# Kernel optimization log

Measured on AMD Instinct MI355X. Metric: run time of the kernel, lower is better.

The kernel has to match this reference:

```python
import jax, jax.numpy as jnp
import numpy as np

N_FEATURES = 512
D_MODEL = 1024
BATCH = 256
LN_EPS = 1e-5


def setup_inputs() -> dict:
    key = jax.random.key(0)
    ks = jax.random.split(key, 8)
    x = jax.random.normal(ks[0], (BATCH, N_FEATURES), dtype=jnp.float32)
    prev_ca = jax.random.uniform(ks[1], (BATCH, D_MODEL), dtype=jnp.float32)
    # phase_proj: Linear(n_features, d_model)
    Wp = jax.random.normal(ks[2], (D_MODEL, N_FEATURES), dtype=jnp.float32) * (1.0 / np.sqrt(N_FEATURES))
    bp = jnp.zeros((D_MODEL,), dtype=jnp.float32)
    # ca_gate: Linear(d_model, d_model//2) + sigmoid
    Wg = jax.random.normal(ks[3], (D_MODEL // 2, D_MODEL), dtype=jnp.float32) * (1.0 / np.sqrt(D_MODEL))
    bg = jnp.zeros((D_MODEL // 2,), dtype=jnp.float32)
    # coupling matrix W (learned param, prev_W is None in default path)
    W = jax.random.normal(ks[4], (D_MODEL, D_MODEL), dtype=jnp.float32) * 0.01
    # LayerNorm params
    gamma = jnp.ones((D_MODEL,), dtype=jnp.float32)
    beta = jnp.zeros((D_MODEL,), dtype=jnp.float32)
    return {"x": x, "prev_ca": prev_ca, "Wp": Wp, "bp": bp, "Wg": Wg, "bg": bg, "W": W, "gamma": gamma, "beta": beta}


def _layernorm(h, gamma, beta):
    mu = jnp.mean(h, axis=-1, keepdims=True)
    var = jnp.mean(jnp.square(h - mu), axis=-1, keepdims=True)
    return (h - mu) * jax.lax.rsqrt(var + LN_EPS) * gamma + beta


def reference(x, prev_ca, Wp, bp, Wg, bg, W, gamma, beta):
    # phi: [B, d]
    phi = x @ Wp.T + bp
    # pairwise phase coherence |cos(phi_i - phi_j)| -> mean over j: [B, d]
    coherence = jnp.abs(jnp.cos(phi[:, :, None] - phi[:, None, :]))  # [B, d, d]
    ca_update = jnp.mean(coherence, axis=2)
    ca = prev_ca * 0.95 + ca_update * 0.05
    # calcium gate: sigmoid(Linear(d -> d//2)), tiled to d
    ca_gate = jax.nn.sigmoid(ca @ Wg.T + bg)  # [B, d//2]
    coupled = phi @ W  # [B, d]
    ca_gate_full = jnp.concatenate([ca_gate, ca_gate], axis=1)  # [B, d]
    features = coupled * ca_gate_full
    features = _layernorm(features + phi, gamma, beta)
    return features, ca, W
```

## Files before the change

kernel.cpp:

```cpp
#include <hip/hip_runtime.h>
#include <math.h>

#define BATCH   256
#define NFEAT   512
#define DMODEL  1024
#define DHALF   512
#define LN_EPS  1e-5f
#define LDSK    68

typedef float f2 __attribute__((ext_vector_type(2)));
typedef float f4 __attribute__((ext_vector_type(4)));

template <int M, int N, int K, int SPLIT, bool B_NT, bool BIAS, bool SIG>
__global__ __launch_bounds__(256) void gemm64_kernel(
    const float* __restrict__ A, const float* __restrict__ B,
    const float* __restrict__ bias, float* __restrict__ C) {
  __shared__ __align__(16) float As[64 * LDSK];
  __shared__ __align__(16) float Bs[64 * LDSK];
  constexpr int KC = K / SPLIT;
  constexpr int NT = KC / 64;
  const int bm  = blockIdx.x * 64;
  const int bn  = blockIdx.y * 64;
  const int kb  = blockIdx.z * KC;
  const int tid = threadIdx.x;
  const int tx  = tid & 15;
  const int ty  = tid >> 4;
  const int r16 = tid >> 4;
  const int c4  = tid & 15;

  f4 ar[4], br[4];

  auto load_tile = [&](int t) {
#pragma unroll
    for (int jj = 0; jj < 4; ++jj) {
      const int row = r16 + jj * 16;
      ar[jj] = *(const f4*)(&A[(size_t)(bm + row) * K + kb + t * 64 + c4 * 4]);
      if (B_NT)
        br[jj] = *(const f4*)(&B[(size_t)(bn + row) * K + kb + t * 64 + c4 * 4]);
      else
        br[jj] = *(const f4*)(&B[(size_t)(kb + t * 64 + row) * N + bn + c4 * 4]);
    }
  };
  auto store_tile = [&]() {
#pragma unroll
    for (int jj = 0; jj < 4; ++jj) {
      const int row = r16 + jj * 16;
      As[(c4 * 4 + 0) * LDSK + row] = ar[jj].x;
      As[(c4 * 4 + 1) * LDSK + row] = ar[jj].y;
      As[(c4 * 4 + 2) * LDSK + row] = ar[jj].z;
      As[(c4 * 4 + 3) * LDSK + row] = ar[jj].w;
      if (B_NT) {
        Bs[(c4 * 4 + 0) * LDSK + row] = br[jj].x;
        Bs[(c4 * 4 + 1) * LDSK + row] = br[jj].y;
        Bs[(c4 * 4 + 2) * LDSK + row] = br[jj].z;
        Bs[(c4 * 4 + 3) * LDSK + row] = br[jj].w;
      } else {
        *(f4*)(&Bs[row * LDSK + c4 * 4]) = br[jj];
      }
    }
  };

  f2 acc[4][2];
#pragma unroll
  for (int i = 0; i < 4; ++i) { acc[i][0] = (f2)0.f; acc[i][1] = (f2)0.f; }

  load_tile(0);
  store_tile();
  __syncthreads();

  for (int t = 0; t < NT; ++t) {
    if (t + 1 < NT) load_tile(t + 1);
#pragma unroll 4
    for (int kk = 0; kk < 64; ++kk) {
      const f4 af = *(const f4*)(&As[kk * LDSK + ty * 4]);
      const f4 bf = *(const f4*)(&Bs[kk * LDSK + tx * 4]);
      const f2 b01 = {bf.x, bf.y};
      const f2 b23 = {bf.z, bf.w};
#pragma unroll
      for (int i = 0; i < 4; ++i) {
        const f2 ai = {af[i], af[i]};
        acc[i][0] += ai * b01;
        acc[i][1] += ai * b23;
      }
    }
    if (t + 1 < NT) {
      __syncthreads();
      store_tile();
      __syncthreads();
    }
  }

  const int z = blockIdx.z;
  f4 bv = {0.f, 0.f, 0.f, 0.f};
  if (BIAS && SPLIT == 1) bv = *(const f4*)(&bias[bn + tx * 4]);
#pragma unroll
  for (int i = 0; i < 4; ++i) {
    const int m = bm + ty * 4 + i;
    f4 cv = {acc[i][0].x, acc[i][0].y, acc[i][1].x, acc[i][1].y};
    if (SPLIT == 1) {
      if (BIAS) cv += bv;
      if (SIG) {
#pragma unroll
        for (int u = 0; u < 4; ++u) cv[u] = 1.f / (1.f + expf(-cv[u]));
      }
      *(f4*)(&C[(size_t)m * N + bn + tx * 4]) = cv;
    } else {
      *(f4*)(&C[((size_t)z * M + m) * N + bn + tx * 4]) = cv;
    }
  }
}

template <int PARTS, bool WRITE_PHI>
__global__ __launch_bounds__(512) void coherence_ca_kernel(
    const float* __restrict__ parts,
    const float* __restrict__ bp, const float* __restrict__ prev_ca,
    float* __restrict__ phi_out, float* __restrict__ ca_out) {
  __shared__ __align__(16) float cc[DMODEL];
  __shared__ __align__(16) float ss[DMODEL];
  const int b   = blockIdx.x;
  const int tid = threadIdx.x;

  f2 ph = ((const f2*)(parts + (size_t)b * DMODEL))[tid];
  if (PARTS > 1) {
#pragma unroll
    for (int z = 1; z < PARTS; ++z)
      ph += ((const f2*)(parts + ((size_t)z * BATCH + b) * DMODEL))[tid];
    ph += ((const f2*)bp)[tid];
    if (WRITE_PHI) ((f2*)(phi_out + (size_t)b * DMODEL))[tid] = ph;
  }
  float ci[2], si[2];
  sincosf(ph.x, &si[0], &ci[0]);
  sincosf(ph.y, &si[1], &ci[1]);
  *(f2*)(&cc[tid * 2]) = f2{ci[0], ci[1]};
  *(f2*)(&ss[tid * 2]) = f2{si[0], si[1]};
  __syncthreads();

  float accA[2] = {0.f, 0.f};
  float accB[2] = {0.f, 0.f};
#pragma unroll 8
  for (int j4 = 0; j4 < DMODEL; j4 += 4) {
    const f4 cy = *(const f4*)(&cc[j4]);
    const f4 sy = *(const f4*)(&ss[j4]);
    const f2 cy01 = {cy.x, cy.y}, cy23 = {cy.z, cy.w};
    const f2 sy01 = {sy.x, sy.y}, sy23 = {sy.z, sy.w};
#pragma unroll
    for (int u = 0; u < 2; ++u) {
      const f2 cu = {ci[u], ci[u]};
      const f2 su = {si[u], si[u]};
      f2 t = su * sy01; t = cu * cy01 + t;
      accA[u] += __builtin_fabsf(t.x);
      accB[u] += __builtin_fabsf(t.y);
      t = su * sy23; t = cu * cy23 + t;
      accA[u] += __builtin_fabsf(t.x);
      accB[u] += __builtin_fabsf(t.y);
    }
  }

  const f2 pc = ((const f2*)(prev_ca + (size_t)b * DMODEL))[tid];
  f2 o;
  o.x = pc.x * 0.95f + (accA[0] + accB[0]) * (0.05f / (float)DMODEL);
  o.y = pc.y * 0.95f + (accA[1] + accB[1]) * (0.05f / (float)DMODEL);
  ((f2*)(ca_out + (size_t)b * DMODEL))[tid] = o;
}

template <int PCP, int PGP, bool GATE_RAW>
__global__ __launch_bounds__(256) void fused_ln_kernel(
    const float* __restrict__ pC, const float* __restrict__ pG,
    const float* __restrict__ phi, const float* __restrict__ bg,
    const float* __restrict__ gamma, const float* __restrict__ beta,
    float* __restrict__ out) {
  __shared__ float red[2][4];
  const int b   = blockIdx.x;
  const int tid = threadIdx.x;
  float gs[2];
#pragma unroll
  for (int h = 0; h < 2; ++h) {
    const int gi = tid + h * 256;
    float s = 0.f;
#pragma unroll
    for (int z = 0; z < PGP; ++z)
      s += pG[((size_t)z * BATCH + b) * DHALF + gi];
    if (GATE_RAW) {
      s += bg[gi];
      s = 1.f / (1.f + expf(-s));
    }
    gs[h] = s;
  }
  float hv[4];
  float sum = 0.f, sumsq = 0.f;
#pragma unroll
  for (int u = 0; u < 4; ++u) {
    const int n = tid + u * 256;
    float cpl = 0.f;
#pragma unroll
    for (int z = 0; z < PCP; ++z)
      cpl += pC[((size_t)z * BATCH + b) * DMODEL + n];
    const float v = fmaf(cpl, gs[u & 1], phi[(size_t)b * DMODEL + n]);
    hv[u] = v;
    sum += v;
    sumsq = fmaf(v, v, sumsq);
  }
  const int lane = tid & 63;
  const int wid  = tid >> 6;
#pragma unroll
  for (int off = 32; off > 0; off >>= 1) {
    sum   += __shfl_down(sum, off);
    sumsq += __shfl_down(sumsq, off);
  }
  if (lane == 0) { red[0][wid] = sum; red[1][wid] = sumsq; }
  __syncthreads();
  sum   = red[0][0] + red[0][1] + red[0][2] + red[0][3];
  sumsq = red[1][0] + red[1][1] + red[1][2] + red[1][3];
  const float mu   = sum * (1.f / DMODEL);
  const float var  = sumsq * (1.f / DMODEL) - mu * mu;
  const float rstd = rsqrtf(var + LN_EPS);
#pragma unroll
  for (int u = 0; u < 4; ++u) {
    const int n = tid + u * 256;
    out[(size_t)b * DMODEL + n] = (hv[u] - mu) * rstd * gamma[n] + beta[n];
  }
}

extern "C" void kernel_launch(void* const* d_in, const int* in_sizes, int n_in,
                              void* d_out, int out_size, void* d_ws,
                              size_t ws_size, hipStream_t stream) {
  const float* x       = (const float*)d_in[0];
  const float* prev_ca = (const float*)d_in[1];
  const float* Wp      = (const float*)d_in[2];
  const float* bp      = (const float*)d_in[3];
  const float* Wg      = (const float*)d_in[4];
  const float* bg      = (const float*)d_in[5];
  const float* W       = (const float*)d_in[6];
  const float* gamma   = (const float*)d_in[7];
  const float* beta    = (const float*)d_in[8];

  float* out_features = (float*)d_out;
  float* out_ca       = out_features + BATCH * DMODEL;
  float* out_W        = out_ca + BATCH * DMODEL;

  const size_t need_main =
      (size_t)(BATCH * DMODEL + 4 * BATCH * DMODEL + 8 * BATCH * DHALF) *
      sizeof(float);
  const size_t need_compact =
      (size_t)(2 * BATCH * DMODEL + BATCH * DHALF) * sizeof(float);

  if (ws_size >= need_main) {
    float* ws   = (float*)d_ws;
    float* phi  = ws;
    float* pbuf = phi + BATCH * DMODEL;
    float* pG   = pbuf + 4 * BATCH * DMODEL;
    gemm64_kernel<BATCH, DMODEL, NFEAT, 4, true, false, false>
        <<<dim3(4, 16, 4), 256, 0, stream>>>(x, Wp, nullptr, pbuf);
    coherence_ca_kernel<4, true><<<BATCH, 512, 0, stream>>>(
        pbuf, bp, prev_ca, phi, out_ca);
    gemm64_kernel<BATCH, DHALF, DMODEL, 8, true, false, false>
        <<<dim3(4, 8, 8), 256, 0, stream>>>(out_ca, Wg, nullptr, pG);
    gemm64_kernel<BATCH, DMODEL, DMODEL, 4, false, false, false>
        <<<dim3(4, 16, 4), 256, 0, stream>>>(phi, W, nullptr, pbuf);
    fused_ln_kernel<4, 8, true><<<BATCH, 256, 0, stream>>>(
        pbuf, pG, phi, bg, gamma, beta, out_features);
  } else {
    float* scratch = (ws_size >= need_compact) ? (float*)d_ws : out_W;
    float* phi     = scratch;
    float* gate    = phi + BATCH * DMODEL;
    float* coupled = gate + BATCH * DHALF;
    gemm64_kernel<BATCH, DMODEL, NFEAT, 1, true, true, false>
        <<<dim3(4, 16, 1), 256, 0, stream>>>(x, Wp, bp, phi);
    coherence_ca_kernel<1, false><<<BATCH, 512, 0, stream>>>(
        phi, bp, prev_ca, nullptr, out_ca);
    gemm64_kernel<BATCH, DHALF, DMODEL, 1, true, true, true>
        <<<dim3(4, 8, 1), 256, 0, stream>>>(out_ca, Wg, bg, gate);
    gemm64_kernel<BATCH, DMODEL, DMODEL, 1, false, false, false>
        <<<dim3(4, 16, 1), 256, 0, stream>>>(phi, W, nullptr, coupled);
    fused_ln_kernel<1, 1, false><<<BATCH, 256, 0, stream>>>(
        coupled, gate, phi, bg, gamma, beta, out_features);
  }

  hipMemcpyAsync(out_W, W, (size_t)DMODEL * DMODEL * sizeof(float),
                 hipMemcpyDeviceToDevice, stream);
}
```

Baseline: 135.7 us.

## Fold W copy into first GEMM launch and double split-K factors

```diff
diff --git a/kernel.cpp b/kernel.cpp
--- a/kernel.cpp
+++ b/kernel.cpp
@@ -11,10 +11,22 @@
 typedef float f2 __attribute__((ext_vector_type(2)));
 typedef float f4 __attribute__((ext_vector_type(4)));
 
-template <int M, int N, int K, int SPLIT, bool B_NT, bool BIAS, bool SIG>
+template <int M, int N, int K, int SPLIT, bool B_NT, bool BIAS, bool SIG,
+          bool COPYW>
 __global__ __launch_bounds__(256) void gemm64_kernel(
     const float* __restrict__ A, const float* __restrict__ B,
-    const float* __restrict__ bias, float* __restrict__ C) {
+    const float* __restrict__ bias, float* __restrict__ C,
+    const f4* __restrict__ cpy_src, f4* __restrict__ cpy_dst) {
+  if (COPYW) {
+    if (blockIdx.z >= (unsigned)SPLIT) {
+      const int cb = (blockIdx.z - SPLIT) * 64 + blockIdx.y * 4 + blockIdx.x;
+      const int base = cb * 2048 + threadIdx.x;
+#pragma unroll
+      for (int k = 0; k < 8; ++k)
+        cpy_dst[base + k * 256] = cpy_src[base + k * 256];
+      return;
+    }
+  }
   __shared__ __align__(16) float As[64 * LDSK];
   __shared__ __align__(16) float Bs[64 * LDSK];
   constexpr int KC = K / SPLIT;
@@ -239,7 +251,7 @@
   float* out_W        = out_ca + BATCH * DMODEL;
 
   const size_t need_main =
-      (size_t)(BATCH * DMODEL + 4 * BATCH * DMODEL + 8 * BATCH * DHALF) *
+      (size_t)(BATCH * DMODEL + 8 * BATCH * DMODEL + 16 * BATCH * DHALF) *
       sizeof(float);
   const size_t need_compact =
       (size_t)(2 * BATCH * DMODEL + BATCH * DHALF) * sizeof(float);
@@ -248,34 +260,38 @@
     float* ws   = (float*)d_ws;
     float* phi  = ws;
     float* pbuf = phi + BATCH * DMODEL;
-    float* pG   = pbuf + 4 * BATCH * DMODEL;
-    gemm64_kernel<BATCH, DMODEL, NFEAT, 4, true, false, false>
-        <<<dim3(4, 16, 4), 256, 0, stream>>>(x, Wp, nullptr, pbuf);
-    coherence_ca_kernel<4, true><<<BATCH, 512, 0, stream>>>(
+    float* pG   = pbuf + 8 * BATCH * DMODEL;
+    gemm64_kernel<BATCH, DMODEL, NFEAT, 8, true, false, false, true>
+        <<<dim3(4, 16, 10), 256, 0, stream>>>(x, Wp, nullptr, pbuf,
+                                              (const f4*)W, (f4*)out_W);
+    coherence_ca_kernel<8, true><<<BATCH, 512, 0, stream>>>(
         pbuf, bp, prev_ca, phi, out_ca);
-    gemm64_kernel<BATCH, DHALF, DMODEL, 8, true, false, false>
-        <<<dim3(4, 8, 8), 256, 0, stream>>>(out_ca, Wg, nullptr, pG);
-    gemm64_kernel<BATCH, DMODEL, DMODEL, 4, false, false, false>
-        <<<dim3(4, 16, 4), 256, 0, stream>>>(phi, W, nullptr, pbuf);
-    fused_ln_kernel<4, 8, true><<<BATCH, 256, 0, stream>>>(
+    gemm64_kernel<BATCH, DHALF, DMODEL, 16, true, false, false, false>
+        <<<dim3(4, 8, 16), 256, 0, stream>>>(out_ca, Wg, nullptr, pG,
+                                             nullptr, nullptr);
+    gemm64_kernel<BATCH, DMODEL, DMODEL, 8, false, false, false, false>
+        <<<dim3(4, 16, 8), 256, 0, stream>>>(phi, W, nullptr, pbuf,
+                                             nullptr, nullptr);
+    fused_ln_kernel<8, 16, true><<<BATCH, 256, 0, stream>>>(
         pbuf, pG, phi, bg, gamma, beta, out_features);
   } else {
     float* scratch = (ws_size >= need_compact) ? (float*)d_ws : out_W;
     float* phi     = scratch;
     float* gate    = phi + BATCH * DMODEL;
     float* coupled = gate + BATCH * DHALF;
-    gemm64_kernel<BATCH, DMODEL, NFEAT, 1, true, true, false>
-        <<<dim3(4, 16, 1), 256, 0, stream>>>(x, Wp, bp, phi);
+    gemm64_kernel<BATCH, DMODEL, NFEAT, 1, true, true, false, false>
+        <<<dim3(4, 16, 1), 256, 0, stream>>>(x, Wp, bp, phi, nullptr, nullptr);
     coherence_ca_kernel<1, false><<<BATCH, 512, 0, stream>>>(
         phi, bp, prev_ca, nullptr, out_ca);
-    gemm64_kernel<BATCH, DHALF, DMODEL, 1, true, true, true>
-        <<<dim3(4, 8, 1), 256, 0, stream>>>(out_ca, Wg, bg, gate);
-    gemm64_kernel<BATCH, DMODEL, DMODEL, 1, false, false, false>
-        <<<dim3(4, 16, 1), 256, 0, stream>>>(phi, W, nullptr, coupled);
+    gemm64_kernel<BATCH, DHALF, DMODEL, 1, true, true, true, false>
+        <<<dim3(4, 8, 1), 256, 0, stream>>>(out_ca, Wg, bg, gate,
+                                            nullptr, nullptr);
+    gemm64_kernel<BATCH, DMODEL, DMODEL, 1, false, false, false, false>
+        <<<dim3(4, 16, 1), 256, 0, stream>>>(phi, W, nullptr, coupled,
+                                             nullptr, nullptr);
     fused_ln_kernel<1, 1, false><<<BATCH, 256, 0, stream>>>(
         coupled, gate, phi, bg, gamma, beta, out_features);
-  }
-
-  hipMemcpyAsync(out_W, W, (size_t)DMODEL * DMODEL * sizeof(float),
-                 hipMemcpyDeviceToDevice, stream);
-}
+    hipMemcpyAsync(out_W, W, (size_t)DMODEL * DMODEL * sizeof(float),
+                   hipMemcpyDeviceToDevice, stream);
+  }
+}
```

New measurement: 131.9 us. 2.8% less time.

## Fuse pipeline into one cooperative persistent kernel with grid syncs

Applied to the files above, without the earlier changes.

```diff
diff --git a/kernel.cpp b/kernel.cpp
--- a/kernel.cpp
+++ b/kernel.cpp
@@ -1,5 +1,8 @@
 #include <hip/hip_runtime.h>
+#include <hip/hip_cooperative_groups.h>
 #include <math.h>
+
+namespace cg = cooperative_groups;
 
 #define BATCH   256
 #define NFEAT   512
@@ -12,22 +15,18 @@
 typedef float f4 __attribute__((ext_vector_type(4)));
 
 template <int M, int N, int K, int SPLIT, bool B_NT, bool BIAS, bool SIG>
-__global__ __launch_bounds__(256) void gemm64_kernel(
+__device__ __forceinline__ void gemm_tile(
     const float* __restrict__ A, const float* __restrict__ B,
-    const float* __restrict__ bias, float* __restrict__ C) {
-  __shared__ __align__(16) float As[64 * LDSK];
-  __shared__ __align__(16) float Bs[64 * LDSK];
+    const float* __restrict__ bias, float* __restrict__ Cp,
+    float* __restrict__ As, float* __restrict__ Bs,
+    const int bx, const int by, const int z, const int tid) {
   constexpr int KC = K / SPLIT;
   constexpr int NT = KC / 64;
-  const int bm  = blockIdx.x * 64;
-  const int bn  = blockIdx.y * 64;
-  const int kb  = blockIdx.z * KC;
-  const int tid = threadIdx.x;
+  const int bm = bx * 64, bn = by * 64, kb = z * KC;
   const int tx  = tid & 15;
   const int ty  = tid >> 4;
   const int r16 = tid >> 4;
   const int c4  = tid & 15;
-
   f4 ar[4], br[4];
 
   auto load_tile = [&](int t) {
@@ -90,7 +89,6 @@
     }
   }
 
-  const int z = blockIdx.z;
   f4 bv = {0.f, 0.f, 0.f, 0.f};
   if (BIAS && SPLIT == 1) bv = *(const f4*)(&bias[bn + tx * 4]);
 #pragma unroll
@@ -103,48 +101,44 @@
 #pragma unroll
         for (int u = 0; u < 4; ++u) cv[u] = 1.f / (1.f + expf(-cv[u]));
       }
-      *(f4*)(&C[(size_t)m * N + bn + tx * 4]) = cv;
+      *(f4*)(&Cp[(size_t)m * N + bn + tx * 4]) = cv;
     } else {
-      *(f4*)(&C[((size_t)z * M + m) * N + bn + tx * 4]) = cv;
+      *(f4*)(&Cp[((size_t)z * M + m) * N + bn + tx * 4]) = cv;
     }
   }
 }
 
 template <int PARTS, bool WRITE_PHI>
-__global__ __launch_bounds__(512) void coherence_ca_kernel(
-    const float* __restrict__ parts,
-    const float* __restrict__ bp, const float* __restrict__ prev_ca,
-    float* __restrict__ phi_out, float* __restrict__ ca_out) {
-  __shared__ __align__(16) float cc[DMODEL];
-  __shared__ __align__(16) float ss[DMODEL];
-  const int b   = blockIdx.x;
-  const int tid = threadIdx.x;
-
-  f2 ph = ((const f2*)(parts + (size_t)b * DMODEL))[tid];
+__device__ __forceinline__ void coherence_row(
+    const float* __restrict__ parts, const float* __restrict__ bp,
+    const float* __restrict__ prev_ca, float* __restrict__ phi_out,
+    float* __restrict__ ca_out, float* __restrict__ cc, float* __restrict__ ss,
+    const int b, const int tid) {
+  f4 ph = ((const f4*)(parts + (size_t)b * DMODEL))[tid];
   if (PARTS > 1) {
 #pragma unroll
     for (int z = 1; z < PARTS; ++z)
-      ph += ((const f2*)(parts + ((size_t)z * BATCH + b) * DMODEL))[tid];
-    ph += ((const f2*)bp)[tid];
-    if (WRITE_PHI) ((f2*)(phi_out + (size_t)b * DMODEL))[tid] = ph;
-  }
-  float ci[2], si[2];
-  sincosf(ph.x, &si[0], &ci[0]);
-  sincosf(ph.y, &si[1], &ci[1]);
-  *(f2*)(&cc[tid * 2]) = f2{ci[0], ci[1]};
-  *(f2*)(&ss[tid * 2]) = f2{si[0], si[1]};
+      ph += ((const f4*)(parts + ((size_t)z * BATCH + b) * DMODEL))[tid];
+    ph += ((const f4*)bp)[tid];
+    if (WRITE_PHI) ((f4*)(phi_out + (size_t)b * DMODEL))[tid] = ph;
+  }
+  float ci[4], si[4];
+#pragma unroll
+  for (int u = 0; u < 4; ++u) { si[u] = __sinf(ph[u]); ci[u] = __cosf(ph[u]); }
+  *(f4*)(&cc[tid * 4]) = f4{ci[0], ci[1], ci[2], ci[3]};
+  *(f4*)(&ss[tid * 4]) = f4{si[0], si[1], si[2], si[3]};
   __syncthreads();
 
-  float accA[2] = {0.f, 0.f};
-  float accB[2] = {0.f, 0.f};
-#pragma unroll 8
+  float accA[4] = {0.f, 0.f, 0.f, 0.f};
+  float accB[4] = {0.f, 0.f, 0.f, 0.f};
+#pragma unroll 4
   for (int j4 = 0; j4 < DMODEL; j4 += 4) {
     const f4 cy = *(const f4*)(&cc[j4]);
     const f4 sy = *(const f4*)(&ss[j4]);
     const f2 cy01 = {cy.x, cy.y}, cy23 = {cy.z, cy.w};
     const f2 sy01 = {sy.x, sy.y}, sy23 = {sy.z, sy.w};
 #pragma unroll
-    for (int u = 0; u < 2; ++u) {
+    for (int u = 0; u < 4; ++u) {
       const f2 cu = {ci[u], ci[u]};
       const f2 su = {si[u], si[u]};
       f2 t = su * sy01; t = cu * cy01 + t;
@@ -155,23 +149,21 @@
       accB[u] += __builtin_fabsf(t.y);
     }
   }
-
-  const f2 pc = ((const f2*)(prev_ca + (size_t)b * DMODEL))[tid];
-  f2 o;
-  o.x = pc.x * 0.95f + (accA[0] + accB[0]) * (0.05f / (float)DMODEL);
-  o.y = pc.y * 0.95f + (accA[1] + accB[1]) * (0.05f / (float)DMODEL);
-  ((f2*)(ca_out + (size_t)b * DMODEL))[tid] = o;
+  const f4 pc = ((const f4*)(prev_ca + (size_t)b * DMODEL))[tid];
+  f4 o;
+#pragma unroll
+  for (int u = 0; u < 4; ++u)
+    o[u] = pc[u] * 0.95f + (accA[u] + accB[u]) * (0.05f / (float)DMODEL);
+  ((f4*)(ca_out + (size_t)b * DMODEL))[tid] = o;
 }
 
 template <int PCP, int PGP, bool GATE_RAW>
-__global__ __launch_bounds__(256) void fused_ln_kernel(
+__device__ __forceinline__ void ln_row(
     const float* __restrict__ pC, const float* __restrict__ pG,
     const float* __restrict__ phi, const float* __restrict__ bg,
     const float* __restrict__ gamma, const float* __restrict__ beta,
-    float* __restrict__ out) {
-  __shared__ float red[2][4];
-  const int b   = blockIdx.x;
-  const int tid = threadIdx.x;
+    float* __restrict__ out, float* __restrict__ red, const int b,
+    const int tid) {
   float gs[2];
 #pragma unroll
   for (int h = 0; h < 2; ++h) {
@@ -207,10 +199,10 @@
     sum   += __shfl_down(sum, off);
     sumsq += __shfl_down(sumsq, off);
   }
-  if (lane == 0) { red[0][wid] = sum; red[1][wid] = sumsq; }
+  if (lane == 0) { red[wid] = sum; red[4 + wid] = sumsq; }
   __syncthreads();
-  sum   = red[0][0] + red[0][1] + red[0][2] + red[0][3];
-  sumsq = red[1][0] + red[1][1] + red[1][2] + red[1][3];
+  sum   = red[0] + red[1] + red[2] + red[3];
+  sumsq = red[4] + red[5] + red[6] + red[7];
   const float mu   = sum * (1.f / DMODEL);
   const float var  = sumsq * (1.f / DMODEL) - mu * mu;
   const float rstd = rsqrtf(var + LN_EPS);
@@ -219,6 +211,88 @@
     const int n = tid + u * 256;
     out[(size_t)b * DMODEL + n] = (hv[u] - mu) * rstd * gamma[n] + beta[n];
   }
+}
+
+__global__ __launch_bounds__(256, 2) void mega_kernel(
+    const float* __restrict__ x, const float* __restrict__ prev_ca,
+    const float* __restrict__ Wp, const float* __restrict__ bp,
+    const float* __restrict__ Wg, const float* __restrict__ bg,
+    const float* __restrict__ W, const float* __restrict__ gamma,
+    const float* __restrict__ beta, float* __restrict__ out_features,
+    float* __restrict__ out_ca, float* __restrict__ out_W,
+    float* __restrict__ phi, float* __restrict__ pbuf,
+    float* __restrict__ pG, float* __restrict__ pC) {
+  __shared__ __align__(16) float lds[2 * 64 * LDSK];
+  float* As = lds;
+  float* Bs = lds + 64 * LDSK;
+  const int gb  = blockIdx.x;
+  const int tid = threadIdx.x;
+  cg::grid_group grid = cg::this_grid();
+
+  {
+    const int z = gb >> 6, rem = gb & 63;
+    gemm_tile<BATCH, DMODEL, NFEAT, 8, true, false, false>(
+        x, Wp, nullptr, pbuf, As, Bs, rem & 3, rem >> 2, z, tid);
+  }
+  grid.sync();
+
+  if (gb < 256) {
+    coherence_row<8, true>(pbuf, bp, prev_ca, phi, out_ca, As, As + DMODEL,
+                           gb, tid);
+  } else {
+    const int base = (gb - 256) * 1024 + tid;
+    const f4* src = (const f4*)W;
+    f4* dst = (f4*)out_W;
+#pragma unroll
+    for (int k = 0; k < 4; ++k) dst[base + k * 256] = src[base + k * 256];
+  }
+  grid.sync();
+
+  if (gb < 256) {
+    const int z = gb >> 5, rem = gb & 31;
+    gemm_tile<BATCH, DHALF, DMODEL, 8, true, false, false>(
+        out_ca, Wg, nullptr, pG, As, Bs, rem & 3, rem >> 2, z, tid);
+  } else {
+    const int g2 = gb - 256;
+    const int z = g2 >> 6, rem = g2 & 63;
+    gemm_tile<BATCH, DMODEL, DMODEL, 4, false, false, false>(
+        phi, W, nullptr, pC, As, Bs, rem & 3, rem >> 2, z, tid);
+  }
+  grid.sync();
+
+  if (gb < 256) {
+    ln_row<4, 8, true>(pC, pG, phi, bg, gamma, beta, out_features, As, gb,
+                       tid);
+  }
+}
+
+template <int M, int N, int K, int SPLIT, bool B_NT, bool BIAS, bool SIG>
+__global__ __launch_bounds__(256) void gemm64_kernel(
+    const float* __restrict__ A, const float* __restrict__ B,
+    const float* __restrict__ bias, float* __restrict__ C) {
+  __shared__ __align__(16) float lds[2 * 64 * LDSK];
+  gemm_tile<M, N, K, SPLIT, B_NT, BIAS, SIG>(A, B, bias, C, lds,
+                                             lds + 64 * LDSK, blockIdx.x,
+                                             blockIdx.y, blockIdx.z,
+                                             threadIdx.x);
+}
+
+__global__ __launch_bounds__(256) void coherence_kernel1(
+    const float* __restrict__ phi, const float* __restrict__ prev_ca,
+    float* __restrict__ ca_out) {
+  __shared__ __align__(16) float lds[2 * DMODEL];
+  coherence_row<1, false>(phi, nullptr, prev_ca, nullptr, ca_out, lds,
+                          lds + DMODEL, blockIdx.x, threadIdx.x);
+}
+
+__global__ __launch_bounds__(256) void ln_kernel1(
+    const float* __restrict__ pC, const float* __restrict__ pG,
+    const float* __restrict__ phi, const float* __restrict__ bg,
+    const float* __restrict__ gamma, const float* __restrict__ beta,
+    float* __restrict__ out) {
+  __shared__ float red[8];
+  ln_row<1, 1, false>(pC, pG, phi, bg, gamma, beta, out, red, blockIdx.x,
+                      threadIdx.x);
 }
 
 extern "C" void kernel_launch(void* const* d_in, const int* in_sizes, int n_in,
@@ -238,44 +312,41 @@
   float* out_ca       = out_features + BATCH * DMODEL;
   float* out_W        = out_ca + BATCH * DMODEL;
 
-  const size_t need_main =
-      (size_t)(BATCH * DMODEL + 4 * BATCH * DMODEL + 8 * BATCH * DHALF) *
-      sizeof(float);
+  float* phi  = (float*)d_ws;
+  float* pbuf = phi + BATCH * DMODEL;
+  float* pG   = pbuf + 8 * BATCH * DMODEL;
+  float* pC   = pG + 8 * BATCH * DHALF;
+
+  const size_t need_mega =
+      (size_t)(BATCH * DMODEL + 8 * BATCH * DMODEL + 8 * BATCH * DHALF +
+               4 * BATCH * DMODEL) * sizeof(float);
   const size_t need_compact =
       (size_t)(2 * BATCH * DMODEL + BATCH * DHALF) * sizeof(float);
 
-  if (ws_size >= need_main) {
-    float* ws   = (float*)d_ws;
-    float* phi  = ws;
-    float* pbuf = phi + BATCH * DMODEL;
-    float* pG   = pbuf + 4 * BATCH * DMODEL;
-    gemm64_kernel<BATCH, DMODEL, NFEAT, 4, true, false, false>
-        <<<dim3(4, 16, 4), 256, 0, stream>>>(x, Wp, nullptr, pbuf);
-    coherence_ca_kernel<4, true><<<BATCH, 512, 0, stream>>>(
-        pbuf, bp, prev_ca, phi, out_ca);
-    gemm64_kernel<BATCH, DHALF, DMODEL, 8, true, false, false>
-        <<<dim3(4, 8, 8), 256, 0, stream>>>(out_ca, Wg, nullptr, pG);
-    gemm64_kernel<BATCH, DMODEL, DMODEL, 4, false, false, false>
-        <<<dim3(4, 16, 4), 256, 0, stream>>>(phi, W, nullptr, pbuf);
-    fused_ln_kernel<4, 8, true><<<BATCH, 256, 0, stream>>>(
-        pbuf, pG, phi, bg, gamma, beta, out_features);
+  if (ws_size >= need_mega) {
+    void* kargs[] = {(void*)&x,   (void*)&prev_ca, (void*)&Wp,
+                     (void*)&bp,  (void*)&Wg,      (void*)&bg,
+                     (void*)&W,   (void*)&gamma,   (void*)&beta,
+                     (void*)&out_features, (void*)&out_ca, (void*)&out_W,
+                     (void*)&phi, (void*)&pbuf,    (void*)&pG,
+                     (void*)&pC};
+    hipLaunchCooperativeKernel((const void*)mega_kernel, dim3(512), dim3(256),
+                               kargs, 0, stream);
   } else {
     float* scratch = (ws_size >= need_compact) ? (float*)d_ws : out_W;
-    float* phi     = scratch;
-    float* gate    = phi + BATCH * DMODEL;
+    float* sphi    = scratch;
+    float* gate    = sphi + BATCH * DMODEL;
     float* coupled = gate + BATCH * DHALF;
     gemm64_kernel<BATCH, DMODEL, NFEAT, 1, true, true, false>
-        <<<dim3(4, 16, 1), 256, 0, stream>>>(x, Wp, bp, phi);
-    coherence_ca_kernel<1, false><<<BATCH, 512, 0, stream>>>(
-        phi, bp, prev_ca, nullptr, out_ca);
+        <<<dim3(4, 16, 1), 256, 0, stream>>>(x, Wp, bp, sphi);
+    coherence_kernel1<<<BATCH, 256, 0, stream>>>(sphi, prev_ca, out_ca);
     gemm64_kernel<BATCH, DHALF, DMODEL, 1, true, true, true>
         <<<dim3(4, 8, 1), 256, 0, stream>>>(out_ca, Wg, bg, gate);
     gemm64_kernel<BATCH, DMODEL, DMODEL, 1, false, false, false>
-        <<<dim3(4, 16, 1), 256, 0, stream>>>(phi, W, nullptr, coupled);
-    fused_ln_kernel<1, 1, false><<<BATCH, 256, 0, stream>>>(
-        coupled, gate, phi, bg, gamma, beta, out_features);
-  }
-
-  hipMemcpyAsync(out_W, W, (size_t)DMODEL * DMODEL * sizeof(float),
-                 hipMemcpyDeviceToDevice, stream);
-}
+        <<<dim3(4, 16, 1), 256, 0, stream>>>(sphi, W, nullptr, coupled);
+    ln_kernel1<<<BATCH, 256, 0, stream>>>(coupled, gate, sphi, bg, gamma,
+                                          beta, out_features);
+    hipMemcpyAsync(out_W, W, (size_t)DMODEL * DMODEL * sizeof(float),
+                   hipMemcpyDeviceToDevice, stream);
+  }
+}
```

Result: slower. 266.2 us (+96.2%).
